# Optimization experiments

Measured on AMD Instinct MI355X. Metric: run time of the kernel, lower is better.

## Reference

```python
import jax, jax.numpy as jnp
import numpy as np

D_MODEL = 512
N = 1024
BS = 64


def setup_inputs() -> dict:
    key = jax.random.key(0)
    ks = jax.random.split(key, 4)
    x = jax.random.normal(ks[0], (BS, N, D_MODEL), dtype=jnp.float32)
    # nn.Linear init per init_weights(): weight ~ N(0, 0.001), bias = 0
    Wq = 0.001 * jax.random.normal(ks[1], (D_MODEL, D_MODEL), dtype=jnp.float32)
    Wk = 0.001 * jax.random.normal(ks[2], (D_MODEL, D_MODEL), dtype=jnp.float32)
    Wv = 0.001 * jax.random.normal(ks[3], (D_MODEL, D_MODEL), dtype=jnp.float32)
    bq = jnp.zeros((D_MODEL,), dtype=jnp.float32)
    bk = jnp.zeros((D_MODEL,), dtype=jnp.float32)
    bv = jnp.zeros((D_MODEL,), dtype=jnp.float32)
    pos_bias = jnp.ones((N, N), dtype=jnp.float32)  # nn.Parameter(ones)
    return {"x": x, "Wq": Wq, "bq": bq, "Wk": Wk, "bk": bk,
            "Wv": Wv, "bv": bv, "pos_bias": pos_bias}


def reference(x, Wq, bq, Wk, bk, Wv, bv, pos_bias):
    # q,k,v: [bs, n, d] via Linear (y = x W^T + b)
    q = jnp.einsum('bnd,ed->bne', x, Wq) + bq
    k = jnp.einsum('bnd,ed->bne', x, Wk) + bk
    v = jnp.einsum('bnd,ed->bne', x, Wv) + bv
    # exp(k[b,j,d] + bias[i,j]) factorizes exactly: exp(bias) * exp(k).
    # This avoids the (n, bs, n, d) broadcast intermediate of the original
    # while computing identical math.
    ek = jnp.exp(k)                                   # [bs, n, d]
    eb = jnp.exp(pos_bias)                            # [n_i, n_j]
    numerator = jnp.einsum('ij,bjd->bid', eb, ek * v)  # sum over j
    denominator = jnp.einsum('ij,bjd->bid', eb, ek)
    out = jax.nn.sigmoid(q) * (numerator / denominator)  # [bs, n, d]
    return out
```

## Files before the change

### kernel.cpp

```cpp
#include <hip/hip_runtime.h>
#include <hip/hip_bf16.h>
#include <stdint.h>


#define NSEQ 1024
#define DM   512

typedef __attribute__((ext_vector_type(8))) short bf16x8;
typedef __attribute__((ext_vector_type(4))) float f32x4;

static __device__ __forceinline__ float b2f(unsigned short u) {
    union { uint32_t i; float f; } c; c.i = ((uint32_t)u) << 16; return c.f;
}
static __device__ __forceinline__ unsigned short f2b(float f) {
    union { float f; uint32_t i; } c; c.f = f;
    uint32_t r = c.i + 0x7FFFu + ((c.i >> 16) & 1u);
    return (unsigned short)(r >> 16);
}
static __device__ __forceinline__ void gl_lds16(const unsigned short* g, unsigned short* l) {
    __builtin_amdgcn_global_load_lds(
        (const __attribute__((address_space(1))) unsigned int*)(g),
        (__attribute__((address_space(3))) unsigned int*)(l), 16, 0, 0);
}

#define PH_BAR() do { asm volatile("" ::: "memory"); \
    __builtin_amdgcn_s_barrier(); asm volatile("" ::: "memory"); } while (0)

__global__ void k_flag0(unsigned int* flag) { *flag = 0u; }

__global__ void k_flag(const float* __restrict__ pb, unsigned int* __restrict__ flag) {
    int i = blockIdx.x * 256 + threadIdx.x;
    float4 v = reinterpret_cast<const float4*>(pb)[i];
    float p0 = pb[0];
    if (v.x != p0 || v.y != p0 || v.z != p0 || v.w != p0) atomicOr(flag, 1u);
}

__global__ void k_eb(const float* __restrict__ pb, unsigned short* __restrict__ eb,
                     const unsigned int* __restrict__ flag) {
    if (*flag == 0u) return;
    int i = blockIdx.x * 256 + threadIdx.x;
    float4 v = reinterpret_cast<const float4*>(pb)[i];
    union { unsigned short u[4]; uint2 p; } o;
    o.u[0] = f2b(__expf(v.x)); o.u[1] = f2b(__expf(v.y));
    o.u[2] = f2b(__expf(v.z)); o.u[3] = f2b(__expf(v.w));
    reinterpret_cast<uint2*>(eb)[i] = o.p;
}

__global__ void k_cvt(const float* __restrict__ src, unsigned short* __restrict__ dst) {
    int i = blockIdx.x * 256 + threadIdx.x;
    const float4* p = reinterpret_cast<const float4*>(src) + (size_t)i * 2;
    float4 f0 = p[0], f1 = p[1];
    union { unsigned short u[8]; int4 v; } o;
    o.u[0]=f2b(f0.x); o.u[1]=f2b(f0.y); o.u[2]=f2b(f0.z); o.u[3]=f2b(f0.w);
    o.u[4]=f2b(f1.x); o.u[5]=f2b(f1.y); o.u[6]=f2b(f1.z); o.u[7]=f2b(f1.w);
    reinterpret_cast<int4*>(dst)[i] = o.v;
}

__global__ void k_cvt_kv(const float* __restrict__ src, unsigned short* __restrict__ Wb,
                         int toff) {
    int i = blockIdx.x * 256 + threadIdx.x;
    int r = i >> 6, c8 = i & 63;
    const float4* p = reinterpret_cast<const float4*>(src + (size_t)r * DM + c8 * 8);
    float4 f0 = p[0], f1 = p[1];
    union { unsigned short u[8]; int4 v; } o;
    o.u[0]=f2b(f0.x); o.u[1]=f2b(f0.y); o.u[2]=f2b(f0.z); o.u[3]=f2b(f0.w);
    o.u[4]=f2b(f1.x); o.u[5]=f2b(f1.y); o.u[6]=f2b(f1.z); o.u[7]=f2b(f1.w);
    int r2 = 512 + ((r >> 6) << 7) + toff + (r & 63);
    *reinterpret_cast<int4*>(&Wb[(size_t)r2 * DM + c8 * 8]) = o.v;
}

template<int NT>
static __device__ __forceinline__ void gemm_p(
    const unsigned short* __restrict__ Abase,
    const unsigned short* __restrict__ Bbase,
    int lda, int ldb, unsigned short* smem, f32x4 (&acc)[8][4],
    int wave, int lane)
{
    const int wr = wave >> 2, wq = wave & 3;
    const int lrow = lane & 15, lkg = lane >> 4;
    const int po  = lane >> 3;
    const int sub = (lane >> 2) & 1;
    const int qp  = lane & 3;

    auto stage = [&](int mat, int s, int h, int t) {
        int p = h * 64 + wave * 8 + po;
        int r = p * 2 + sub;
        int q = qp ^ (p & 3);
        int col = ((t & (NT - 1)) << 5) + q * 8;
        const unsigned short* g = (mat ? Bbase + (size_t)r * ldb
                                       : Abase + (size_t)r * lda) + col;
        unsigned short* d = smem + mat * 32768 + s * 8192 + (h * 64 + wave * 8) * 64;
        gl_lds16(g, d);
    };
    auto loadA = [&](int s, int h, bf16x8* af) {
        const unsigned short* base = smem + s * 8192;
        #pragma unroll
        for (int mi = 0; mi < 4; ++mi) {
            int r = wr * 128 + h * 64 + mi * 16 + lrow;
            int p = r >> 1;
            af[mi] = *reinterpret_cast<const bf16x8*>(
                base + p * 64 + (r & 1) * 32 + ((lkg ^ (p & 3)) << 3));
        }
    };
    auto loadB = [&](int s, bf16x8* bf) {
        const unsigned short* base = smem + 32768 + s * 8192;
        #pragma unroll
        for (int ni = 0; ni < 4; ++ni) {
            int r = wq * 64 + ni * 16 + lrow;
            int p = r >> 1;
            bf[ni] = *reinterpret_cast<const bf16x8*>(
                base + p * 64 + (r & 1) * 32 + ((lkg ^ (p & 3)) << 3));
        }
    };
    auto mfma16 = [&](int h, bf16x8* af, bf16x8* bf) {
        __builtin_amdgcn_s_setprio(1);
        #pragma unroll
        for (int mi = 0; mi < 4; ++mi)
            #pragma unroll
            for (int ni = 0; ni < 4; ++ni)
                acc[h * 4 + mi][ni] = __builtin_amdgcn_mfma_f32_16x16x32_bf16(
                    af[mi], bf[ni], acc[h * 4 + mi][ni], 0, 0, 0);
        __builtin_amdgcn_s_setprio(0);
    };

    #pragma unroll
    for (int pt = 0; pt < 3; ++pt) {
        stage(0, pt, 0, pt); stage(0, pt, 1, pt);
        stage(1, pt, 0, pt); stage(1, pt, 1, pt);
    }
    asm volatile("s_waitcnt vmcnt(8)" ::: "memory");
    __builtin_amdgcn_s_barrier();

    #pragma unroll 1
    for (int tt = 0; tt < NT; tt += 4) {
        #pragma unroll
        for (int u = 0; u < 4; ++u) {
            const int t = tt + u;
            const int s = u, s3 = (u + 3) & 3, t3 = t + 3;
            bf16x8 af[4], bfr[4];
            loadB(s, bfr); loadA(s, 0, af);
            stage(0, s3, 0, t3); stage(0, s3, 1, t3);
            mfma16(0, af, bfr);
            loadA(s, 1, af);
            stage(1, s3, 0, t3); stage(1, s3, 1, t3);
            mfma16(1, af, bfr);
            asm volatile("s_waitcnt vmcnt(8)" ::: "memory");
            __builtin_amdgcn_s_barrier();
        }
    }
    asm volatile("s_waitcnt vmcnt(0)" ::: "memory");
    __builtin_amdgcn_s_barrier();
}

__launch_bounds__(512)
__global__ void k_qkv(const unsigned short* __restrict__ xb,
                      const unsigned short* __restrict__ Wb,
                      const float* __restrict__ bq, const float* __restrict__ bk,
                      const float* __restrict__ bv,
                      unsigned short* __restrict__ s_out,
                      unsigned short* __restrict__ Z,
                      float* __restrict__ P,
                      const unsigned int* __restrict__ flag)
{
    extern __shared__ unsigned short smem[];
    const int bid = blockIdx.x;
    const int logical = (bid & 7) * 192 + (bid >> 3);
    const int mtile = logical / 6, etile = logical % 6;
    const int brow = mtile * 256;
    const int erow = etile * 256;
    const bool isq = (etile < 2);
    const bool uni = (*flag == 0u);

    const int tid = threadIdx.x;
    const int lane = tid & 63, wave = tid >> 6;
    const int wr = wave >> 2, wq = wave & 3;
    const int lrow = lane & 15, lkg = lane >> 4;

    f32x4 acc[8][4];
    const f32x4 z4 = {0.f, 0.f, 0.f, 0.f};
    #pragma unroll
    for (int a = 0; a < 8; ++a)
        #pragma unroll
        for (int c = 0; c < 4; ++c) acc[a][c] = z4;

    gemm_p<16>(xb + (size_t)brow * DM, Wb + (size_t)erow * DM, DM, DM,
               smem, acc, wave, lane);

    unsigned short* T = smem;
    if (isq) {
        const int ecol = etile * 256;
        #pragma unroll
        for (int pp = 0; pp < 2; ++pp) {
            __syncthreads();
            if ((wq >> 1) == pp) {
                #pragma unroll
                for (int mi = 0; mi < 8; ++mi) {
                    int m0 = wr*128 + mi*16 + lkg*4;
                    #pragma unroll
                    for (int ni = 0; ni < 4; ++ni) {
                        int nl = (wq & 1) * 64 + ni*16 + lrow;
                        float bia = bq[ecol + pp*128 + nl];
                        #pragma unroll
                        for (int r = 0; r < 4; ++r) {
                            float tq = acc[mi][ni][r] + bia;
                            float sg = __builtin_amdgcn_rcpf(1.f + __expf(-tq));
                            T[(m0 + r) * 136 + nl] = f2b(sg);
                        }
                    }
                }
            }
            __syncthreads();
            #pragma unroll
            for (int it = 0; it < 8; ++it) {
                int idx = it * 512 + tid;
                int m = idx >> 4, ng = idx & 15;
                int4 vv = *reinterpret_cast<const int4*>(&T[m * 136 + ng * 8]);
                *reinterpret_cast<int4*>(
                    &s_out[(size_t)(brow + m) * DM + ecol + pp*128 + ng * 8]) = vv;
            }
        }
    } else {
        const int gbase = (etile - 2) * 2;
        const int b = brow >> 10;
        const int jtile = (brow >> 8) & 3;
        float psum[8];
        #pragma unroll
        for (int it = 0; it < 8; ++it) psum[it] = 0.f;

        #pragma unroll
        for (int pp = 0; pp < 2; ++pp) {
            __syncthreads();
            if (wr == pp) {
                #pragma unroll
                for (int mi = 0; mi < 8; ++mi) {
                    int m0 = mi*16 + lkg*4;
                    #pragma unroll
                    for (int ni = 0; ni < 4; ++ni) {
                        int n = wq*64 + ni*16 + lrow;
                        int sub = (n >> 6) & 1, dr = n & 63;
                        int d = (gbase + (n >> 7)) * 64 + dr;
                        float bia = (sub == 0) ? bk[d] : bv[d];
                        union { unsigned short u[4]; uint2 p; } o;
                        #pragma unroll
                        for (int r = 0; r < 4; ++r) {
                            float tv = acc[mi][ni][r] + bia;
                            o.u[r] = f2b((sub == 0) ? __expf(tv) : tv);
                        }
                        *reinterpret_cast<uint2*>(&T[n * 136 + m0]) = o.p;
                    }
                }
            }
            __syncthreads();
            const int j0 = (brow & (NSEQ - 1)) + pp * 128;
            #pragma unroll
            for (int it = 0; it < 8; ++it) {
                int idx = it * 512 + tid;
                int zr = idx >> 4, jg = idx & 15;
                int gg = zr >> 7, sub2 = (zr >> 6) & 1, dr = zr & 63;
                int d = (gbase + gg) * 64 + dr;
                union { unsigned short u[8]; int4 v; } o;
                if (sub2 == 0) {
                    union { unsigned short u[8]; int4 v; } pe, pv;
                    pe.v = *reinterpret_cast<const int4*>(&T[(gg*128 + dr) * 136 + jg*8]);
                    pv.v = *reinterpret_cast<const int4*>(&T[(gg*128 + 64 + dr) * 136 + jg*8]);
                    #pragma unroll
                    for (int j = 0; j < 8; ++j) o.u[j] = f2b(b2f(pe.u[j]) * b2f(pv.u[j]));
                } else {
                    o.v = *reinterpret_cast<const int4*>(&T[(gg*128 + dr) * 136 + jg*8]);
                }
                if (uni) {
                    float sv = 0.f;
                    #pragma unroll
                    for (int j = 0; j < 8; ++j) sv += b2f(o.u[j]);
                    sv += __shfl_xor(sv, 1);
                    sv += __shfl_xor(sv, 2);
                    sv += __shfl_xor(sv, 4);
                    sv += __shfl_xor(sv, 8);
                    psum[it] += sv;
                } else {
                    int nn = ((d >> 4) << 5) + sub2 * 16 + (d & 15);
                    size_t off = ((size_t)(b * NSEQ + nn)) * NSEQ + j0 + jg * 8;
                    *reinterpret_cast<int4*>(&Z[off]) = o.v;
                }
            }
        }
        if (uni) {
            #pragma unroll
            for (int it = 0; it < 8; ++it) {
                int idx = it * 512 + tid;
                int zr = idx >> 4, jg = idx & 15;
                if (jg == 0) {
                    int gg = zr >> 7, sub2 = (zr >> 6) & 1, dr = zr & 63;
                    int d = (gbase + gg) * 64 + dr;
                    P[sub2 * 131072 + b * 2048 + jtile * 512 + d] = psum[it];
                }
            }
        }
    }
}

__launch_bounds__(256)
__global__ void k_sum2(const float* __restrict__ P,
                       const unsigned int* __restrict__ flag,
                       float* __restrict__ R)
{
    if (*flag != 0u) return;
    int gid = blockIdx.x * 256 + threadIdx.x;
    int b = gid >> 9, d = gid & 511;
    const float* p0 = P + b * 2048 + d;
    const float* p1 = P + 131072 + b * 2048 + d;
    float num = p0[0] + p0[512] + p0[1024] + p0[1536];
    float den = p1[0] + p1[512] + p1[1024] + p1[1536];
    R[gid] = num / den;
}

__launch_bounds__(256)
__global__ void k_out(const unsigned short* __restrict__ s_in,
                      const float* __restrict__ R,
                      const unsigned int* __restrict__ flag,
                      float* __restrict__ out)
{
    if (*flag != 0u) return;
    int idx = blockIdx.x * 256 + threadIdx.x;
    int row = idx >> 6;
    int d0 = (idx & 63) * 8;
    int b = row >> 10;
    union { unsigned short u[8]; int4 v; } sv;
    sv.v = *reinterpret_cast<const int4*>(&s_in[(size_t)row * DM + d0]);
    const float4* rp = reinterpret_cast<const float4*>(&R[b * 512 + d0]);
    float4 r0 = rp[0], r1 = rp[1];
    float4 o0, o1;
    o0.x = b2f(sv.u[0]) * r0.x; o0.y = b2f(sv.u[1]) * r0.y;
    o0.z = b2f(sv.u[2]) * r0.z; o0.w = b2f(sv.u[3]) * r0.w;
    o1.x = b2f(sv.u[4]) * r1.x; o1.y = b2f(sv.u[5]) * r1.y;
    o1.z = b2f(sv.u[6]) * r1.z; o1.w = b2f(sv.u[7]) * r1.w;
    float4* op = reinterpret_cast<float4*>(&out[(size_t)row * DM + d0]);
    op[0] = o0; op[1] = o1;
}

__launch_bounds__(512)
__global__ void k_aft(const unsigned short* __restrict__ eb,
                      const unsigned short* __restrict__ Z,
                      const unsigned short* __restrict__ s_in,
                      const unsigned int* __restrict__ flag,
                      float* __restrict__ out)
{
    if (*flag == 0u) return;
    extern __shared__ unsigned short smem[];
    const int bid = blockIdx.x;
    const int logical = (bid & 7) * 32 + (bid >> 3);
    const int itile = logical & 3, ncol = logical >> 2;
    const int i0 = itile * 256;

    const int tid = threadIdx.x;
    const int lane = tid & 63, wave = tid >> 6;
    const int wr = wave >> 2, wq = wave & 3;
    const int lrow = lane & 15, lkg = lane >> 4;
    const int po = lane >> 3, sub = (lane >> 2) & 1, qp = lane & 3;
    const int ch0 = wave * 2;

    const unsigned short* Abase = eb + (size_t)i0 * NSEQ;
    const unsigned short* Bbase = Z + (size_t)ncol * 4 * 256 * NSEQ;

    f32x4 acc[8][4];
    const f32x4 z4 = {0.f, 0.f, 0.f, 0.f};
    #pragma unroll
    for (int a = 0; a < 8; ++a)
        #pragma unroll
        for (int c = 0; c < 4; ++c) acc[a][c] = z4;

    auto half = [&](int isB, int d, int c) -> unsigned short* {
        return smem + isB * 32768 + (d * 2 + c) * 8192;
    };
    auto stg = [&](int isB, int d, int c, int t) {
        int ta = t & 63, gp = ta >> 4, tk = ta & 15;
        unsigned short* dst = half(isB, d, c);
        #pragma unroll
        for (int q2 = 0; q2 < 2; ++q2) {
            int ch = ch0 + q2;
            int p = ch * 8 + po, r = p * 2 + sub;
            int col = (tk << 6) + (c << 5) + ((qp ^ (p & 3)) << 3);
            const unsigned short* g = isB
                ? Bbase + ((size_t)(gp * 256 + r)) * NSEQ + col
                : Abase + (size_t)r * NSEQ + col;
            gl_lds16(g, dst + ch * 512);
        }
    };
    auto ldA = [&](int d, int c, int h, bf16x8* af) {
        const unsigned short* base = half(0, d, c);
        #pragma unroll
        for (int mi = 0; mi < 4; ++mi) {
            int r = wr * 128 + h * 64 + mi * 16 + lrow, p = r >> 1;
            af[mi] = *reinterpret_cast<const bf16x8*>(
                base + p * 64 + (r & 1) * 32 + ((lkg ^ (p & 3)) << 3));
        }
    };
    auto ldB = [&](int d, int c, bf16x8* bf) {
        const unsigned short* base = half(1, d, c);
        #pragma unroll
        for (int ni = 0; ni < 4; ++ni) {
            int r = wq * 64 + ni * 16 + lrow, p = r >> 1;
            bf[ni] = *reinterpret_cast<const bf16x8*>(
                base + p * 64 + (r & 1) * 32 + ((lkg ^ (p & 3)) << 3));
        }
    };
    auto mm = [&](int h, bf16x8* af, bf16x8* bf) {
        __builtin_amdgcn_s_setprio(1);
        #pragma unroll
        for (int mi = 0; mi < 4; ++mi)
            #pragma unroll
            for (int ni = 0; ni < 4; ++ni)
                acc[h * 4 + mi][ni] = __builtin_amdgcn_mfma_f32_16x16x32_bf16(
                    af[mi], bf[ni], acc[h * 4 + mi][ni], 0, 0, 0);
        __builtin_amdgcn_s_setprio(0);
    };

    stg(0, 0, 0, 0); stg(1, 0, 0, 0);
    stg(0, 0, 1, 0); stg(1, 0, 1, 0);
    stg(0, 1, 0, 1); stg(1, 1, 0, 1);
    asm volatile("s_waitcnt vmcnt(4)" ::: "memory");
    __builtin_amdgcn_s_barrier();
    asm volatile("" ::: "memory");

    #pragma unroll 1
    for (int g = 0; g < 4; ++g) {
        #pragma unroll 1
        for (int ii = 0; ii < 8; ++ii) {
            const int T = (g << 4) + (ii << 1);
            const int U = T + 1, T2 = T + 2, U2 = T + 3;
            bf16x8 af[4], bf[4];
            ldB(0, 0, bf); ldA(0, 0, 0, af); stg(0, 1, 1, U);
            PH_BAR(); mm(0, af, bf); PH_BAR();
            ldA(0, 0, 1, af); stg(1, 1, 1, U);
            PH_BAR(); mm(1, af, bf); PH_BAR();
            ldB(0, 1, bf); ldA(0, 1, 0, af); stg(0, 0, 0, T2);
            PH_BAR(); mm(0, af, bf); PH_BAR();
            ldA(0, 1, 1, af); stg(1, 0, 0, T2);
            asm volatile("s_waitcnt vmcnt(4)" ::: "memory");
            PH_BAR(); mm(1, af, bf); PH_BAR();
            ldB(1, 0, bf); ldA(1, 0, 0, af); stg(0, 0, 1, T2);
            PH_BAR(); mm(0, af, bf); PH_BAR();
            ldA(1, 0, 1, af); stg(1, 0, 1, T2);
            PH_BAR(); mm(1, af, bf); PH_BAR();
            ldB(1, 1, bf); ldA(1, 1, 0, af); stg(0, 1, 0, U2);
            PH_BAR(); mm(0, af, bf); PH_BAR();
            ldA(1, 1, 1, af); stg(1, 1, 0, U2);
            asm volatile("s_waitcnt vmcnt(4)" ::: "memory");
            PH_BAR(); mm(1, af, bf); PH_BAR();
        }
        const int n0 = (ncol * 4 + g) * 256;
        #pragma unroll
        for (int mi = 0; mi < 8; ++mi) {
            int i = i0 + wr*128 + mi*16 + lkg*4;
            #pragma unroll
            for (int pi = 0; pi < 2; ++pi) {
                int nA = n0 + wq*64 + pi*32 + lrow;
                int b  = nA >> 10, nn = nA & (NSEQ - 1);
                int d  = ((nn >> 5) << 4) + (nn & 15);
                #pragma unroll
                for (int r = 0; r < 4; ++r) {
                    size_t o = ((size_t)(b * NSEQ + i + r)) * DM + d;
                    out[o] = b2f(s_in[o]) * acc[mi][pi*2][r] / acc[mi][pi*2 + 1][r];
                }
                acc[mi][pi*2] = z4; acc[mi][pi*2 + 1] = z4;
            }
        }
    }
    asm volatile("s_waitcnt vmcnt(0)" ::: "memory");
}

extern "C" void kernel_launch(void* const* d_in, const int* in_sizes, int n_in,
                              void* d_out, int out_size, void* d_ws, size_t ws_size,
                              hipStream_t stream)
{
    const float* x  = (const float*)d_in[0];
    const float* Wq = (const float*)d_in[1];
    const float* bq = (const float*)d_in[2];
    const float* Wk = (const float*)d_in[3];
    const float* bk = (const float*)d_in[4];
    const float* Wv = (const float*)d_in[5];
    const float* bv = (const float*)d_in[6];
    const float* pb = (const float*)d_in[7];
    float* out = (float*)d_out;

    char* ws = (char*)d_ws;
    unsigned short* eb   = (unsigned short*)(ws);
    float*          Pbuf = (float*)(ws);
    unsigned short* Wb   = (unsigned short*)(ws + ((size_t)2 << 20));
    unsigned int*   flag = (unsigned int*)(ws + 0x380000);
    float*          Rbuf = (float*)(ws + 0x384000);
    unsigned short* xb   = (unsigned short*)(ws + ((size_t)4   << 20));
    unsigned short* s    = (unsigned short*)(ws + ((size_t)68  << 20));
    unsigned short* Z    = (unsigned short*)(ws + ((size_t)132 << 20));

    k_flag0<<<1, 1, 0, stream>>>(flag);
    k_flag<<<1024, 256, 0, stream>>>(pb, flag);
    k_eb <<<1024, 256, 0, stream>>>(pb, eb, flag);
    k_cvt<<<16384, 256, 0, stream>>>(x,  xb);
    k_cvt<<<128,   256, 0, stream>>>(Wq, Wb);
    k_cvt_kv<<<128, 256, 0, stream>>>(Wk, Wb, 0);
    k_cvt_kv<<<128, 256, 0, stream>>>(Wv, Wb, 64);
    k_qkv<<<1536, 512, 131072, stream>>>(xb, Wb, bq, bk, bv, s, Z, Pbuf, flag);
    k_sum2<<<128, 256, 0, stream>>>(Pbuf, flag, Rbuf);
    k_out<<<16384, 256, 0, stream>>>(s, Rbuf, flag, out);
    k_aft<<<256, 512, 131072, stream>>>(eb, Z, s, flag, out);
}
```

Measured before the change: 234.4 us.

## Split QKV GEMM into KV-reduce and Q kernels, fusing output scaling into Q

The combined QKV GEMM is split into two kernels. The K/V kernel interleaves K and V weight rows so each lane pair holds matching exp(k) and v values, and reduces the column sums straight from registers through shuffles instead of staging through LDS. The Q kernel runs after the ratio reduction and writes sigmoid(q)*R straight to the output, which removes the bf16 intermediate round trip and the separate elementwise kernel. The cost is one more GEMM launch and serialising the Q GEMM after the K/V reduction.

```diff
diff --git a/kernel.cpp b/kernel.cpp
--- a/kernel.cpp
+++ b/kernel.cpp
@@ -65,7 +65,7 @@
     union { unsigned short u[8]; int4 v; } o;
     o.u[0]=f2b(f0.x); o.u[1]=f2b(f0.y); o.u[2]=f2b(f0.z); o.u[3]=f2b(f0.w);
     o.u[4]=f2b(f1.x); o.u[5]=f2b(f1.y); o.u[6]=f2b(f1.z); o.u[7]=f2b(f1.w);
-    int r2 = 512 + ((r >> 6) << 7) + toff + (r & 63);
+    int r2 = 512 + ((r >> 7) << 8) + ((r & 127) << 1) + toff;
     *reinterpret_cast<int4*>(&Wb[(size_t)r2 * DM + c8 * 8]) = o.v;
 }
 
@@ -153,22 +153,19 @@
 }
 
 __launch_bounds__(512)
-__global__ void k_qkv(const unsigned short* __restrict__ xb,
-                      const unsigned short* __restrict__ Wb,
-                      const float* __restrict__ bq, const float* __restrict__ bk,
-                      const float* __restrict__ bv,
-                      unsigned short* __restrict__ s_out,
-                      unsigned short* __restrict__ Z,
-                      float* __restrict__ P,
-                      const unsigned int* __restrict__ flag)
+__global__ void k_kv(const unsigned short* __restrict__ xb,
+                     const unsigned short* __restrict__ Wb,
+                     const float* __restrict__ bk, const float* __restrict__ bv,
+                     unsigned short* __restrict__ Z,
+                     float* __restrict__ P,
+                     const unsigned int* __restrict__ flag)
 {
     extern __shared__ unsigned short smem[];
     const int bid = blockIdx.x;
-    const int logical = (bid & 7) * 192 + (bid >> 3);
-    const int mtile = logical / 6, etile = logical % 6;
+    const int logical = (bid & 7) * 128 + (bid >> 3);
+    const int mtile = logical >> 2, e4 = logical & 3;
     const int brow = mtile * 256;
-    const int erow = etile * 256;
-    const bool isq = (etile < 2);
+    const int b = brow >> 10, jtile = (brow >> 8) & 3;
     const bool uni = (*flag == 0u);
 
     const int tid = threadIdx.x;
@@ -183,50 +180,52 @@
         #pragma unroll
         for (int c = 0; c < 4; ++c) acc[a][c] = z4;
 
-    gemm_p<16>(xb + (size_t)brow * DM, Wb + (size_t)erow * DM, DM, DM,
+    gemm_p<16>(xb + (size_t)brow * DM, Wb + (size_t)(512 + e4 * 256) * DM, DM, DM,
                smem, acc, wave, lane);
 
-    unsigned short* T = smem;
-    if (isq) {
-        const int ecol = etile * 256;
-        #pragma unroll
-        for (int pp = 0; pp < 2; ++pp) {
-            __syncthreads();
-            if ((wq >> 1) == pp) {
+    if (uni) {
+        const int sub = lrow & 1;
+        float* SF = reinterpret_cast<float*>(smem);
+        float se[4], sv2[4];
+        #pragma unroll
+        for (int ni = 0; ni < 4; ++ni) {
+            int n = wq * 64 + ni * 16 + lrow;
+            int d = e4 * 128 + (n >> 1);
+            float bia = sub ? bv[d] : bk[d];
+            float accv = 0.f, acce = 0.f;
+            #pragma unroll
+            for (int mi = 0; mi < 8; ++mi) {
                 #pragma unroll
-                for (int mi = 0; mi < 8; ++mi) {
-                    int m0 = wr*128 + mi*16 + lkg*4;
-                    #pragma unroll
-                    for (int ni = 0; ni < 4; ++ni) {
-                        int nl = (wq & 1) * 64 + ni*16 + lrow;
-                        float bia = bq[ecol + pp*128 + nl];
-                        #pragma unroll
-                        for (int r = 0; r < 4; ++r) {
-                            float tq = acc[mi][ni][r] + bia;
-                            float sg = __builtin_amdgcn_rcpf(1.f + __expf(-tq));
-                            T[(m0 + r) * 136 + nl] = f2b(sg);
-                        }
-                    }
+                for (int r = 0; r < 4; ++r) {
+                    float val = acc[mi][ni][r] + bia;
+                    float e = sub ? val : __expf(val);
+                    float partner = __shfl_xor(e, 1);
+                    if (!sub) { accv += e * partner; acce += e; }
                 }
             }
-            __syncthreads();
-            #pragma unroll
-            for (int it = 0; it < 8; ++it) {
-                int idx = it * 512 + tid;
-                int m = idx >> 4, ng = idx & 15;
-                int4 vv = *reinterpret_cast<const int4*>(&T[m * 136 + ng * 8]);
-                *reinterpret_cast<int4*>(
-                    &s_out[(size_t)(brow + m) * DM + ecol + pp*128 + ng * 8]) = vv;
-            }
+            accv += __shfl_xor(accv, 16); accv += __shfl_xor(accv, 32);
+            acce += __shfl_xor(acce, 16); acce += __shfl_xor(acce, 32);
+            se[ni] = acce; sv2[ni] = accv;
+        }
+        __syncthreads();
+        if (sub == 0 && lkg == 0) {
+            #pragma unroll
+            for (int ni = 0; ni < 4; ++ni) {
+                int dl = wq * 32 + ni * 8 + (lrow >> 1);
+                SF[wr * 256 + dl * 2]     = sv2[ni];
+                SF[wr * 256 + dl * 2 + 1] = se[ni];
+            }
+        }
+        __syncthreads();
+        if (tid < 128) {
+            int dl = tid, d = e4 * 128 + dl;
+            float num = SF[dl * 2]     + SF[256 + dl * 2];
+            float den = SF[dl * 2 + 1] + SF[256 + dl * 2 + 1];
+            P[b * 2048 + jtile * 512 + d] = num;
+            P[131072 + b * 2048 + jtile * 512 + d] = den;
         }
     } else {
-        const int gbase = (etile - 2) * 2;
-        const int b = brow >> 10;
-        const int jtile = (brow >> 8) & 3;
-        float psum[8];
-        #pragma unroll
-        for (int it = 0; it < 8; ++it) psum[it] = 0.f;
-
+        unsigned short* T = smem;
         #pragma unroll
         for (int pp = 0; pp < 2; ++pp) {
             __syncthreads();
@@ -237,14 +236,14 @@
                     #pragma unroll
                     for (int ni = 0; ni < 4; ++ni) {
                         int n = wq*64 + ni*16 + lrow;
-                        int sub = (n >> 6) & 1, dr = n & 63;
-                        int d = (gbase + (n >> 7)) * 64 + dr;
-                        float bia = (sub == 0) ? bk[d] : bv[d];
+                        int sub = n & 1;
+                        int d = e4 * 128 + (n >> 1);
+                        float bia = sub ? bv[d] : bk[d];
                         union { unsigned short u[4]; uint2 p; } o;
                         #pragma unroll
                         for (int r = 0; r < 4; ++r) {
                             float tv = acc[mi][ni][r] + bia;
-                            o.u[r] = f2b((sub == 0) ? __expf(tv) : tv);
+                            o.u[r] = f2b(sub ? tv : __expf(tv));
                         }
                         *reinterpret_cast<uint2*>(&T[n * 136 + m0]) = o.p;
                     }
@@ -256,44 +255,21 @@
             for (int it = 0; it < 8; ++it) {
                 int idx = it * 512 + tid;
                 int zr = idx >> 4, jg = idx & 15;
-                int gg = zr >> 7, sub2 = (zr >> 6) & 1, dr = zr & 63;
-                int d = (gbase + gg) * 64 + dr;
+                int t = zr >> 7, dli = zr & 127;
+                int d = e4 * 128 + dli;
                 union { unsigned short u[8]; int4 v; } o;
-                if (sub2 == 0) {
+                if (t == 0) {
                     union { unsigned short u[8]; int4 v; } pe, pv;
-                    pe.v = *reinterpret_cast<const int4*>(&T[(gg*128 + dr) * 136 + jg*8]);
-                    pv.v = *reinterpret_cast<const int4*>(&T[(gg*128 + 64 + dr) * 136 + jg*8]);
+                    pe.v = *reinterpret_cast<const int4*>(&T[(2*dli)     * 136 + jg*8]);
+                    pv.v = *reinterpret_cast<const int4*>(&T[(2*dli + 1) * 136 + jg*8]);
                     #pragma unroll
                     for (int j = 0; j < 8; ++j) o.u[j] = f2b(b2f(pe.u[j]) * b2f(pv.u[j]));
                 } else {
-                    o.v = *reinterpret_cast<const int4*>(&T[(gg*128 + dr) * 136 + jg*8]);
+                    o.v = *reinterpret_cast<const int4*>(&T[(2*dli) * 136 + jg*8]);
                 }
-                if (uni) {
-                    float sv = 0.f;
-                    #pragma unroll
-                    for (int j = 0; j < 8; ++j) sv += b2f(o.u[j]);
-                    sv += __shfl_xor(sv, 1);
-                    sv += __shfl_xor(sv, 2);
-                    sv += __shfl_xor(sv, 4);
-                    sv += __shfl_xor(sv, 8);
-                    psum[it] += sv;
-                } else {
-                    int nn = ((d >> 4) << 5) + sub2 * 16 + (d & 15);
-                    size_t off = ((size_t)(b * NSEQ + nn)) * NSEQ + j0 + jg * 8;
-                    *reinterpret_cast<int4*>(&Z[off]) = o.v;
-                }
-            }
-        }
-        if (uni) {
-            #pragma unroll
-            for (int it = 0; it < 8; ++it) {
-                int idx = it * 512 + tid;
-                int zr = idx >> 4, jg = idx & 15;
-                if (jg == 0) {
-                    int gg = zr >> 7, sub2 = (zr >> 6) & 1, dr = zr & 63;
-                    int d = (gbase + gg) * 64 + dr;
-                    P[sub2 * 131072 + b * 2048 + jtile * 512 + d] = psum[it];
-                }
+                int nz = ((d >> 4) << 5) + t * 16 + (d & 15);
+                size_t off = ((size_t)(b * NSEQ + nz)) * NSEQ + j0 + jg * 8;
+                *reinterpret_cast<int4*>(&Z[off]) = o.v;
             }
         }
     }
@@ -314,28 +290,91 @@
     R[gid] = num / den;
 }
 
-__launch_bounds__(256)
-__global__ void k_out(const unsigned short* __restrict__ s_in,
-                      const float* __restrict__ R,
-                      const unsigned int* __restrict__ flag,
-                      float* __restrict__ out)
+__launch_bounds__(512)
+__global__ void k_q(const unsigned short* __restrict__ xb,
+                    const unsigned short* __restrict__ Wb,
+                    const float* __restrict__ bq,
+                    const float* __restrict__ R,
+                    unsigned short* __restrict__ s_out,
+                    float* __restrict__ out,
+                    const unsigned int* __restrict__ flag)
 {
-    if (*flag != 0u) return;
-    int idx = blockIdx.x * 256 + threadIdx.x;
-    int row = idx >> 6;
-    int d0 = (idx & 63) * 8;
-    int b = row >> 10;
-    union { unsigned short u[8]; int4 v; } sv;
-    sv.v = *reinterpret_cast<const int4*>(&s_in[(size_t)row * DM + d0]);
-    const float4* rp = reinterpret_cast<const float4*>(&R[b * 512 + d0]);
-    float4 r0 = rp[0], r1 = rp[1];
-    float4 o0, o1;
-    o0.x = b2f(sv.u[0]) * r0.x; o0.y = b2f(sv.u[1]) * r0.y;
-    o0.z = b2f(sv.u[2]) * r0.z; o0.w = b2f(sv.u[3]) * r0.w;
-    o1.x = b2f(sv.u[4]) * r1.x; o1.y = b2f(sv.u[5]) * r1.y;
-    o1.z = b2f(sv.u[6]) * r1.z; o1.w = b2f(sv.u[7]) * r1.w;
-    float4* op = reinterpret_cast<float4*>(&out[(size_t)row * DM + d0]);
-    op[0] = o0; op[1] = o1;
+    extern __shared__ unsigned short smem[];
+    const int bid = blockIdx.x;
+    const int logical = (bid & 7) * 64 + (bid >> 3);
+    const int mtile = logical >> 1, etile = logical & 1;
+    const int brow = mtile * 256;
+    const int ecol = etile * 256;
+    const int b = brow >> 10;
+    const bool uni = (*flag == 0u);
+
+    const int tid = threadIdx.x;
+    const int lane = tid & 63, wave = tid >> 6;
+    const int wr = wave >> 2, wq = wave & 3;
+    const int lrow = lane & 15, lkg = lane >> 4;
+
+    f32x4 acc[8][4];
+    const f32x4 z4 = {0.f, 0.f, 0.f, 0.f};
+    #pragma unroll
+    for (int a = 0; a < 8; ++a)
+        #pragma unroll
+        for (int c = 0; c < 4; ++c) acc[a][c] = z4;
+
+    gemm_p<16>(xb + (size_t)brow * DM, Wb + (size_t)ecol * DM, DM, DM,
+               smem, acc, wave, lane);
+
+    unsigned short* T = smem;
+    #pragma unroll
+    for (int pp = 0; pp < 2; ++pp) {
+        __syncthreads();
+        if ((wq >> 1) == pp) {
+            #pragma unroll
+            for (int mi = 0; mi < 8; ++mi) {
+                int m0 = wr*128 + mi*16 + lkg*4;
+                #pragma unroll
+                for (int ni = 0; ni < 4; ++ni) {
+                    int nl = (wq & 1) * 64 + ni*16 + lrow;
+                    float bia = bq[ecol + pp*128 + nl];
+                    #pragma unroll
+                    for (int r = 0; r < 4; ++r) {
+                        float tq = acc[mi][ni][r] + bia;
+                        float sg = __builtin_amdgcn_rcpf(1.f + __expf(-tq));
+                        T[(m0 + r) * 136 + nl] = f2b(sg);
+                    }
+                }
+            }
+        }
+        __syncthreads();
+        if (uni) {
+            #pragma unroll
+            for (int it = 0; it < 8; ++it) {
+                int idx = it * 512 + tid;
+                int m = idx >> 4, ng = idx & 15;
+                union { unsigned short u[8]; int4 v; } sv;
+                sv.v = *reinterpret_cast<const int4*>(&T[m * 136 + ng * 8]);
+                int dcol = ecol + pp * 128 + ng * 8;
+                const float4* rp = reinterpret_cast<const float4*>(&R[b * 512 + dcol]);
+                float4 r0 = rp[0], r1 = rp[1];
+                float4 o0, o1;
+                o0.x = b2f(sv.u[0]) * r0.x; o0.y = b2f(sv.u[1]) * r0.y;
+                o0.z = b2f(sv.u[2]) * r0.z; o0.w = b2f(sv.u[3]) * r0.w;
+                o1.x = b2f(sv.u[4]) * r1.x; o1.y = b2f(sv.u[5]) * r1.y;
+                o1.z = b2f(sv.u[6]) * r1.z; o1.w = b2f(sv.u[7]) * r1.w;
+                float4* op = reinterpret_cast<float4*>(
+                    &out[(size_t)(brow + m) * DM + dcol]);
+                op[0] = o0; op[1] = o1;
+            }
+        } else {
+            #pragma unroll
+            for (int it = 0; it < 8; ++it) {
+                int idx = it * 512 + tid;
+                int m = idx >> 4, ng = idx & 15;
+                int4 vv = *reinterpret_cast<const int4*>(&T[m * 136 + ng * 8]);
+                *reinterpret_cast<int4*>(
+                    &s_out[(size_t)(brow + m) * DM + ecol + pp*128 + ng * 8]) = vv;
+            }
+        }
+    }
 }
 
 __launch_bounds__(512)
@@ -499,9 +538,9 @@
     k_cvt<<<16384, 256, 0, stream>>>(x,  xb);
     k_cvt<<<128,   256, 0, stream>>>(Wq, Wb);
     k_cvt_kv<<<128, 256, 0, stream>>>(Wk, Wb, 0);
-    k_cvt_kv<<<128, 256, 0, stream>>>(Wv, Wb, 64);
-    k_qkv<<<1536, 512, 131072, stream>>>(xb, Wb, bq, bk, bv, s, Z, Pbuf, flag);
+    k_cvt_kv<<<128, 256, 0, stream>>>(Wv, Wb, 1);
+    k_kv<<<1024, 512, 131072, stream>>>(xb, Wb, bk, bv, Z, Pbuf, flag);
     k_sum2<<<128, 256, 0, stream>>>(Pbuf, flag, Rbuf);
-    k_out<<<16384, 256, 0, stream>>>(s, Rbuf, flag, out);
+    k_q<<<512, 512, 131072, stream>>>(xb, Wb, bq, Rbuf, s, out, flag);
     k_aft<<<256, 512, 131072, stream>>>(eb, Z, s, flag, out);
 }
```

Result: faster. 212.8 us (-9.3%).
